# Optimization experiments

Hardware: AMD Instinct MI355X
Metric: run time of the kernel (lower is better)

The kernel has to match this reference:

```python
import jax, jax.numpy as jnp
import numpy as np

B, S, DIN, DOUT = 4, 4096, 768, 768

def setup_inputs() -> dict:
    key = jax.random.key(0)
    kx, kq, kk, kv = jax.random.split(key, 4)
    scale = 1.0 / np.sqrt(DIN)
    return {
        "x": jax.random.normal(kx, (B, S, DIN), dtype=jnp.float32),
        "Wq": jax.random.normal(kq, (DIN, DOUT), dtype=jnp.float32) * scale,
        "Wk": jax.random.normal(kk, (DIN, DOUT), dtype=jnp.float32) * scale,
        "Wv": jax.random.normal(kv, (DIN, DOUT), dtype=jnp.float32) * scale,
    }

def reference(x, Wq, Wk, Wv):
    # q,k,v: [B,S,DOUT]
    q = jnp.einsum('bsd,de->bse', x, Wq)
    k = jnp.einsum('bsd,de->bse', x, Wk)
    v = jnp.einsum('bsd,de->bse', x, Wv)
    # scores: [B,S,S], causal mask (upper triangle -> -inf)
    scores = jnp.einsum('bqe,bke->bqk', q, k)
    causal = jnp.tril(jnp.ones((S, S), dtype=bool))  # True where allowed
    scores = jnp.where(causal[None, :, :], scores, -jnp.inf)
    weights = jax.nn.softmax(scores / jnp.sqrt(jnp.float32(DOUT)), axis=-1)
    # dropout_rate = 0.0 -> identity
    return jnp.einsum('bqk,bke->bqe', weights, v)
```

## Files before the change

kernel.cpp:

```cpp
#include <hip/hip_runtime.h>
#include <math.h>


typedef unsigned short u16;
typedef unsigned int u32;
typedef __attribute__((ext_vector_type(8))) __bf16 bf8;
typedef __attribute__((ext_vector_type(4))) float f32x4;

struct __align__(8) U4 { u16 x, y, z, w; };

#define LOG2E 1.4426950408889634f
#define QSCALE 0.03608439182435161f

#define SBAR() __builtin_amdgcn_s_barrier()
#define WAIT_LGKM0() asm volatile("s_waitcnt lgkmcnt(0)" ::: "memory")
#define WAIT_VM4() asm volatile("s_waitcnt vmcnt(4)" ::: "memory")
#define WAIT_VM0() asm volatile("s_waitcnt vmcnt(0)" ::: "memory")

__device__ __forceinline__ u16 f2bf(float f) {
  u32 u = __builtin_bit_cast(u32, f);
  u += 0x7FFFu + ((u >> 16) & 1u);
  return (u16)(u >> 16);
}
__device__ __forceinline__ f32x4 mfma16(bf8 a, bf8 b, f32x4 c) {
  return __builtin_amdgcn_mfma_f32_16x16x32_bf16(a, b, c, 0, 0, 0);
}
__device__ __forceinline__ void stage16(const void* g, void* l) {
  __builtin_amdgcn_global_load_lds((const __attribute__((address_space(1))) void*)g,
                                   (__attribute__((address_space(3))) void*)l, 16, 0, 0);
}
__device__ __forceinline__ u32 swz7(u32 off) { return off ^ (((off >> 7) & 7u) << 4); }

__global__ void cvt_x_kernel(const float* __restrict__ x, u16* __restrict__ xb) {
  int i = blockIdx.x * 256 + threadIdx.x;
  float4 v = ((const float4*)x)[i];
  U4 o; o.x = f2bf(v.x); o.y = f2bf(v.y); o.z = f2bf(v.z); o.w = f2bf(v.w);
  ((U4*)xb)[i] = o;
}

__global__ void cvt_w_kernel(const float* __restrict__ Wq, const float* __restrict__ Wk,
                             const float* __restrict__ Wv, u16* __restrict__ wt) {
  __shared__ float tile[32][33];
  int z = blockIdx.z;
  const float* W = (z == 0) ? Wq : ((z == 1) ? Wk : Wv);
  u16* o = wt + (size_t)z * 589824;
  int n0 = blockIdx.x * 32, k0 = blockIdx.y * 32;
  int c = threadIdx.x & 31, r0 = threadIdx.x >> 5;
#pragma unroll
  for (int p = 0; p < 4; p++) tile[r0 + p * 8][c] = W[(size_t)(k0 + r0 + p * 8) * 768 + n0 + c];
  __syncthreads();
#pragma unroll
  for (int p = 0; p < 4; p++) o[(size_t)(n0 + r0 + p * 8) * 768 + k0 + c] = f2bf(tile[c][r0 + p * 8]);
}

__global__ __launch_bounds__(256) void gemm_qkv_kernel(
    const u16* __restrict__ xb, const u16* __restrict__ wt,
    u16* __restrict__ qo, u16* __restrict__ ko, u16* __restrict__ vT) {
  __shared__ char lA[16384];
  __shared__ char lB[16384];
  const int tid = threadIdx.x;
  const int lane = tid & 63, wvid = tid >> 6;
  const int wm = wvid >> 1, wn = wvid & 1;
  const int l15 = lane & 15, lg4 = lane >> 4;
  const int m0 = blockIdx.x * 128;
  const int n0 = blockIdx.y * 128;
  const int z = blockIdx.z;
  const u16* wz = wt + (size_t)z * 589824;

  f32x4 acc[4][4];
#pragma unroll
  for (int rt = 0; rt < 4; rt++)
#pragma unroll
    for (int nt = 0; nt < 4; nt++) acc[rt][nt] = f32x4{0.f, 0.f, 0.f, 0.f};

  for (int kt = 0; kt < 12; kt++) {
#pragma unroll
    for (int i = 0; i < 4; i++) {
      u32 o = (u32)i * 4096u + (u32)wvid * 1024u + (u32)lane * 16u;
      u32 lg = swz7(o);
      u32 row = lg >> 7, kbyt = lg & 127u;
      stage16((const char*)xb + ((size_t)(m0 + row) * 1536 + (size_t)kt * 128 + kbyt),
              lA + (size_t)i * 4096 + (size_t)wvid * 1024);
      stage16((const char*)wz + ((size_t)(n0 + row) * 1536 + (size_t)kt * 128 + kbyt),
              lB + (size_t)i * 4096 + (size_t)wvid * 1024);
    }
    __syncthreads();
#pragma unroll
    for (int kk = 0; kk < 2; kk++) {
      bf8 af[4], bfr[4];
#pragma unroll
      for (int rt = 0; rt < 4; rt++) {
        u32 off = (u32)(wm * 64 + rt * 16 + l15) * 128u + (u32)kk * 64u + (u32)lg4 * 16u;
        af[rt] = *(const bf8*)(const void*)(lA + swz7(off));
      }
#pragma unroll
      for (int nt = 0; nt < 4; nt++) {
        u32 off = (u32)(wn * 64 + nt * 16 + l15) * 128u + (u32)kk * 64u + (u32)lg4 * 16u;
        bfr[nt] = *(const bf8*)(const void*)(lB + swz7(off));
      }
#pragma unroll
      for (int rt = 0; rt < 4; rt++)
#pragma unroll
        for (int nt = 0; nt < 4; nt++) acc[rt][nt] = mfma16(af[rt], bfr[nt], acc[rt][nt]);
    }
    __syncthreads();
  }
  if (z == 2) {
#pragma unroll
    for (int rt = 0; rt < 4; rt++) {
      int m = m0 + wm * 64 + rt * 16 + lg4 * 4;
      int batch = m >> 12;
      int s = m & 4095;
#pragma unroll
      for (int nt = 0; nt < 4; nt++) {
        int col = n0 + wn * 64 + nt * 16 + l15;
        U4 pk;
        pk.x = f2bf(acc[rt][nt][0]); pk.y = f2bf(acc[rt][nt][1]);
        pk.z = f2bf(acc[rt][nt][2]); pk.w = f2bf(acc[rt][nt][3]);
        *(U4*)(vT + ((size_t)batch * 768 + col) * 4096 + s) = pk;
      }
    }
  } else {
    u16* dst = (z == 0) ? qo : ko;
    float scl = (z == 0) ? QSCALE : 1.0f;
#pragma unroll
    for (int rt = 0; rt < 4; rt++)
#pragma unroll
      for (int nt = 0; nt < 4; nt++) {
        int col = n0 + wn * 64 + nt * 16 + l15;
#pragma unroll
        for (int j = 0; j < 4; j++) {
          int m = m0 + wm * 64 + rt * 16 + lg4 * 4 + j;
          dst[(size_t)m * 768 + col] = f2bf(acc[rt][nt][j] * scl);
        }
      }
  }
}

__global__ __attribute__((amdgpu_flat_work_group_size(512, 512)))
__attribute__((amdgpu_waves_per_eu(2, 2))) void attn_kernel(
    const u16* __restrict__ qg, const u16* __restrict__ kg, const u16* __restrict__ vg,
    float* __restrict__ out) {
  __shared__ char Qlds[49152];
  __shared__ char Klds[3][32768];
  __shared__ char Plds[8192];
  __shared__ float pm[2][4][16];
  __shared__ float ps[2][4][16];
  __shared__ float mrun[32], lrun[32], alpha_s[32];

  const int tid = threadIdx.x;
  const int lane = tid & 63;
  const int wv = tid >> 6;
  const int rg = wv >> 2;
  const int cg = wv & 3;
  const int l15 = lane & 15, lg4 = lane >> 4;

  const int b = blockIdx.x;
  const int batch = (b >> 1) & 3;
  const int qb_i = 127 - (((b >> 3) << 1) + (b & 1));
  const int qbase = qb_i * 32;
  const size_t boff = (size_t)batch * 4096;
  const int ntile = (qb_i >> 2) + 1;
  const int gtot = ntile * 6;

  const u16* kbase = kg + boff * 768;

  u32 soff[4];
#pragma unroll
  for (int p = 0; p < 4; p++) {
    u32 o = (u32)p * 8192u + (u32)tid * 16u;
    u32 key = o >> 8;
    u32 dbyte = (o & 255u) ^ ((key & 7u) << 4);
    soff[p] = key * 768u + (dbyte >> 1);
  }

#pragma unroll
  for (int p = 0; p < 4; p++)
    stage16(kbase + soff[p], &Klds[0][p * 8192 + tid * 16]);
#pragma unroll
  for (int p = 0; p < 4; p++)
    stage16(kbase + soff[p] + 128u, &Klds[1][p * 8192 + tid * 16]);

#pragma unroll
  for (int j = 0; j < 6; j++) {
    int li = j * 512 + tid;
    int row = li / 96;
    int c16 = li - row * 96;
    int tt = c16 >> 2, sl = c16 & 3;
    u32 daddr = (u32)tt * 2048u + (u32)row * 64u + (u32)((sl ^ ((row >> 1) & 3)) << 4);
    bf8 v = *(const bf8*)(const void*)(qg + (boff + qbase + row) * 768 + c16 * 8);
    *(bf8*)(void*)(Qlds + daddr) = v;
  }
  if (tid < 32) { mrun[tid] = -INFINITY; lrun[tid] = 0.f; }
  WAIT_LGKM0(); SBAR();

  const int qrow_loc = rg * 16 + l15;
  const u32 qlds_base = (u32)qrow_loc * 64u + (u32)((lg4 ^ ((qrow_loc >> 1) & 3)) << 4);
  const u32 kxm = (u32)(l15 & 7) << 4;
  const u32 pa_col = ((u32)lg4 * 16u) ^ ((u32)(l15 & 3) << 4);
  const u32 pa_kx = (u32)((l15 >> 2) & 1);

  f32x4 acc[2][6];
#pragma unroll
  for (int rt = 0; rt < 2; rt++)
#pragma unroll
    for (int ct = 0; ct < 6; ct++) acc[rt][ct] = f32x4{0.f, 0.f, 0.f, 0.f};

  for (int kt = 0; kt < ntile; kt++) {
    const int kb = kt * 128;
    f32x4 sv0 = f32x4{0.f, 0.f, 0.f, 0.f}, sv1 = sv0;

#pragma unroll
    for (int c = 0; c < 6; c++) {
      const int g = kt * 6 + c;
      if (g + 1 < gtot) { WAIT_VM4(); } else { WAIT_VM0(); }
      SBAR();
      {
        const char* kbuf = Klds[c % 3];
#pragma unroll
        for (int ks = 0; ks < 4; ks++) {
          bf8 qv = *(const bf8*)(const void*)(Qlds + qlds_base + (u32)(c * 4 + ks) * 2048u);
          u32 inr = ((u32)ks * 64u + (u32)lg4 * 16u) ^ kxm;
          bf8 kv0 = *(const bf8*)(const void*)(kbuf + (u32)(cg * 32 + l15) * 256u + inr);
          bf8 kv1 = *(const bf8*)(const void*)(kbuf + (u32)(cg * 32 + 16 + l15) * 256u + inr);
          sv0 = mfma16(qv, kv0, sv0);
          sv1 = mfma16(qv, kv1, sv1);
        }
      }
      WAIT_LGKM0(); SBAR();
      if (g + 2 < gtot) {
        const int g2 = g + 2;
        const int kt1 = g2 / 6, c1 = g2 - kt1 * 6;
        const u16* src = kbase + (size_t)(kt1 * 128) * 768 + c1 * 128;
        char* dstb = &Klds[(c + 2) % 3][0];
#pragma unroll
        for (int p = 0; p < 4; p++)
          stage16(src + soff[p], dstb + p * 8192 + tid * 16);
      }
    }

    if (kt == ntile - 1) {
      const int rowg = qbase + rg * 16 + lg4 * 4;
      const int col0 = kb + cg * 32 + l15;
#pragma unroll
      for (int j = 0; j < 4; j++) {
        if (col0 > rowg + j) sv0[j] = -INFINITY;
        if (col0 + 16 > rowg + j) sv1[j] = -INFINITY;
      }
    }
    float rmax[4];
#pragma unroll
    for (int j = 0; j < 4; j++) {
      float m = fmaxf(sv0[j], sv1[j]);
      m = fmaxf(m, __shfl_xor(m, 1));
      m = fmaxf(m, __shfl_xor(m, 2));
      m = fmaxf(m, __shfl_xor(m, 4));
      m = fmaxf(m, __shfl_xor(m, 8));
      rmax[j] = m;
    }
    if (l15 == 0) {
#pragma unroll
      for (int j = 0; j < 4; j++) pm[rg][cg][lg4 * 4 + j] = rmax[j];
    }
    WAIT_LGKM0(); SBAR();
    if (tid < 32) {
      int r2 = tid >> 4, ix = tid & 15;
      float mo = mrun[tid];
      float mn = fmaxf(fmaxf(pm[r2][0][ix], pm[r2][1][ix]), fmaxf(pm[r2][2][ix], pm[r2][3][ix]));
      mn = fmaxf(mo, mn);
      alpha_s[tid] = exp2f((mo - mn) * LOG2E);
      mrun[tid] = mn;
    }
    WAIT_LGKM0(); SBAR();
    {
      float psum[4];
      const int prow0 = rg * 16 + lg4 * 4;
#pragma unroll
      for (int j = 0; j < 4; j++) {
        int r = prow0 + j;
        float mrow = mrun[r];
        float p0 = exp2f((sv0[j] - mrow) * LOG2E);
        float p1 = exp2f((sv1[j] - mrow) * LOG2E);
        u32 rb = (u32)r * 256u;
        u32 msk = (u32)(r & 7) << 4;
        *(u16*)(void*)(Plds + rb + (((u32)(cg * 32 + l15) * 2u) ^ msk)) = f2bf(p0);
        *(u16*)(void*)(Plds + rb + (((u32)(cg * 32 + 16 + l15) * 2u) ^ msk)) = f2bf(p1);
        float su = p0 + p1;
        su += __shfl_xor(su, 1);
        su += __shfl_xor(su, 2);
        su += __shfl_xor(su, 4);
        su += __shfl_xor(su, 8);
        psum[j] = su;
      }
      if (l15 == 0) {
#pragma unroll
        for (int j = 0; j < 4; j++) ps[rg][cg][lg4 * 4 + j] = psum[j];
      }
    }
    const u16* vb0 = vg + ((size_t)batch * 768 + wv * 96 + l15) * 4096 + kb + lg4 * 8;
    bf8 vcur0, vcur1, vcur2, vcur3, vcur4, vcur5;
    vcur0 = *(const bf8*)(const void*)(vb0);
    vcur1 = *(const bf8*)(const void*)(vb0 + 65536);
    vcur2 = *(const bf8*)(const void*)(vb0 + 131072);
    vcur3 = *(const bf8*)(const void*)(vb0 + 196608);
    vcur4 = *(const bf8*)(const void*)(vb0 + 262144);
    vcur5 = *(const bf8*)(const void*)(vb0 + 327680);
    {
      float al[8];
#pragma unroll
      for (int rt = 0; rt < 2; rt++)
#pragma unroll
        for (int j = 0; j < 4; j++) al[rt * 4 + j] = alpha_s[rt * 16 + lg4 * 4 + j];
#pragma unroll
      for (int ct = 0; ct < 6; ct++)
#pragma unroll
        for (int rt = 0; rt < 2; rt++)
#pragma unroll
          for (int j = 0; j < 4; j++) acc[rt][ct][j] *= al[rt * 4 + j];
    }
    WAIT_LGKM0(); SBAR();
    if (tid < 32) {
      int r2 = tid >> 4, ix = tid & 15;
      lrun[tid] = lrun[tid] * alpha_s[tid] +
                  ps[r2][0][ix] + ps[r2][1][ix] + ps[r2][2][ix] + ps[r2][3][ix];
    }
#pragma unroll
    for (int ks = 0; ks < 4; ks++) {
      u32 kss = ((u32)ks ^ pa_kx) * 64u;
      bf8 pa0 = *(const bf8*)(const void*)(Plds + (u32)l15 * 256u + pa_col + kss);
      bf8 pa1 = *(const bf8*)(const void*)(Plds + ((u32)l15 * 256u + 4096u) + pa_col + kss);
      bf8 vn0, vn1, vn2, vn3, vn4, vn5;
      if (ks < 3) {
        const u16* vnp = vb0 + (ks + 1) * 32;
        vn0 = *(const bf8*)(const void*)(vnp);
        vn1 = *(const bf8*)(const void*)(vnp + 65536);
        vn2 = *(const bf8*)(const void*)(vnp + 131072);
        vn3 = *(const bf8*)(const void*)(vnp + 196608);
        vn4 = *(const bf8*)(const void*)(vnp + 262144);
        vn5 = *(const bf8*)(const void*)(vnp + 327680);
      }
      acc[0][0] = mfma16(pa0, vcur0, acc[0][0]);  acc[1][0] = mfma16(pa1, vcur0, acc[1][0]);
      acc[0][1] = mfma16(pa0, vcur1, acc[0][1]);  acc[1][1] = mfma16(pa1, vcur1, acc[1][1]);
      acc[0][2] = mfma16(pa0, vcur2, acc[0][2]);  acc[1][2] = mfma16(pa1, vcur2, acc[1][2]);
      acc[0][3] = mfma16(pa0, vcur3, acc[0][3]);  acc[1][3] = mfma16(pa1, vcur3, acc[1][3]);
      acc[0][4] = mfma16(pa0, vcur4, acc[0][4]);  acc[1][4] = mfma16(pa1, vcur4, acc[1][4]);
      acc[0][5] = mfma16(pa0, vcur5, acc[0][5]);  acc[1][5] = mfma16(pa1, vcur5, acc[1][5]);
      if (ks < 3) {
        vcur0 = vn0; vcur1 = vn1; vcur2 = vn2; vcur3 = vn3; vcur4 = vn4; vcur5 = vn5;
      }
    }
  }
  WAIT_LGKM0(); SBAR();
  float inv[8];
#pragma unroll
  for (int rt = 0; rt < 2; rt++)
#pragma unroll
    for (int j = 0; j < 4; j++) inv[rt * 4 + j] = 1.f / lrun[rt * 16 + lg4 * 4 + j];
#pragma unroll
  for (int ct = 0; ct < 6; ct++)
#pragma unroll
    for (int rt = 0; rt < 2; rt++)
#pragma unroll
      for (int j = 0; j < 4; j++) {
        size_t o = (boff + (size_t)(qbase + rt * 16 + lg4 * 4 + j)) * 768 + wv * 96 + ct * 16 + l15;
        out[o] = acc[rt][ct][j] * inv[rt * 4 + j];
      }
}

extern "C" void kernel_launch(void* const* d_in, const int* in_sizes, int n_in,
                              void* d_out, int out_size, void* d_ws, size_t ws_size,
                              hipStream_t stream) {
  const float* x  = (const float*)d_in[0];
  const float* Wq = (const float*)d_in[1];
  const float* Wk = (const float*)d_in[2];
  const float* Wv = (const float*)d_in[3];
  float* out = (float*)d_out;

  char* ws = (char*)d_ws;
  u16* xb = (u16*)(ws + 256);
  u16* qb = xb + 12582912;
  u16* kb = qb + 12582912;
  u16* vT = kb + 12582912;
  u16* wt = vT + 12582912;

  cvt_x_kernel<<<12288, 256, 0, stream>>>(x, xb);
  cvt_w_kernel<<<dim3(24, 24, 3), 256, 0, stream>>>(Wq, Wk, Wv, wt);
  gemm_qkv_kernel<<<dim3(128, 6, 3), 256, 0, stream>>>(xb, wt, qb, kb, vT);
  attn_kernel<<<512, 512, 0, stream>>>(qb, kb, vT, out);
}
```

Measured before the change: 550.1 us.

## Use 32x32 MFMA for PV, keep Q in registers, widen K chunks

Measured after the change: 611.3 us. 1.11x slower.

```diff
diff --git a/kernel.cpp b/kernel.cpp
--- a/kernel.cpp
+++ b/kernel.cpp
@@ -6,6 +6,7 @@
 typedef unsigned int u32;
 typedef __attribute__((ext_vector_type(8))) __bf16 bf8;
 typedef __attribute__((ext_vector_type(4))) float f32x4;
+typedef __attribute__((ext_vector_type(16))) float f32x16;
 
 struct __align__(8) U4 { u16 x, y, z, w; };
 
@@ -14,7 +15,8 @@
 
 #define SBAR() __builtin_amdgcn_s_barrier()
 #define WAIT_LGKM0() asm volatile("s_waitcnt lgkmcnt(0)" ::: "memory")
-#define WAIT_VM4() asm volatile("s_waitcnt vmcnt(4)" ::: "memory")
+#define WAIT_VM18() asm volatile("s_waitcnt vmcnt(18)" ::: "memory")
+#define WAIT_VM6() asm volatile("s_waitcnt vmcnt(6)" ::: "memory")
 #define WAIT_VM0() asm volatile("s_waitcnt vmcnt(0)" ::: "memory")
 
 __device__ __forceinline__ u16 f2bf(float f) {
@@ -24,6 +26,9 @@
 }
 __device__ __forceinline__ f32x4 mfma16(bf8 a, bf8 b, f32x4 c) {
   return __builtin_amdgcn_mfma_f32_16x16x32_bf16(a, b, c, 0, 0, 0);
+}
+__device__ __forceinline__ f32x16 mfma32(bf8 a, bf8 b, f32x16 c) {
+  return __builtin_amdgcn_mfma_f32_32x32x16_bf16(a, b, c, 0, 0, 0);
 }
 __device__ __forceinline__ void stage16(const void* g, void* l) {
   __builtin_amdgcn_global_load_lds((const __attribute__((address_space(1))) void*)g,
@@ -141,12 +146,11 @@
 __attribute__((amdgpu_waves_per_eu(2, 2))) void attn_kernel(
     const u16* __restrict__ qg, const u16* __restrict__ kg, const u16* __restrict__ vg,
     float* __restrict__ out) {
-  __shared__ char Qlds[49152];
-  __shared__ char Klds[3][32768];
+  __shared__ char Klds[3][49152];
   __shared__ char Plds[8192];
   __shared__ float pm[2][4][16];
   __shared__ float ps[2][4][16];
-  __shared__ float mrun[32], lrun[32], alpha_s[32];
+  __shared__ float mrun_s[32], alpha_s2[32], lrun_s[32];
 
   const int tid = threadIdx.x;
   const int lane = tid & 63;
@@ -154,6 +158,7 @@
   const int rg = wv >> 2;
   const int cg = wv & 3;
   const int l15 = lane & 15, lg4 = lane >> 4;
+  const int l31 = lane & 31, lh = lane >> 5;
 
   const int b = blockIdx.x;
   const int batch = (b >> 1) & 3;
@@ -161,81 +166,78 @@
   const int qbase = qb_i * 32;
   const size_t boff = (size_t)batch * 4096;
   const int ntile = (qb_i >> 2) + 1;
-  const int gtot = ntile * 6;
+  const int gtot = ntile * 4;
 
   const u16* kbase = kg + boff * 768;
 
-  u32 soff[4];
-#pragma unroll
-  for (int p = 0; p < 4; p++) {
+  u32 soff[6];
+#pragma unroll
+  for (int p = 0; p < 6; p++) {
     u32 o = (u32)p * 8192u + (u32)tid * 16u;
-    u32 key = o >> 8;
-    u32 dbyte = (o & 255u) ^ ((key & 7u) << 4);
-    soff[p] = key * 768u + (dbyte >> 1);
-  }
-
-#pragma unroll
-  for (int p = 0; p < 4; p++)
-    stage16(kbase + soff[p], &Klds[0][p * 8192 + tid * 16]);
-#pragma unroll
-  for (int p = 0; p < 4; p++)
-    stage16(kbase + soff[p] + 128u, &Klds[1][p * 8192 + tid * 16]);
-
-#pragma unroll
-  for (int j = 0; j < 6; j++) {
-    int li = j * 512 + tid;
-    int row = li / 96;
-    int c16 = li - row * 96;
-    int tt = c16 >> 2, sl = c16 & 3;
-    u32 daddr = (u32)tt * 2048u + (u32)row * 64u + (u32)((sl ^ ((row >> 1) & 3)) << 4);
-    bf8 v = *(const bf8*)(const void*)(qg + (boff + qbase + row) * 768 + c16 * 8);
-    *(bf8*)(void*)(Qlds + daddr) = v;
-  }
-  if (tid < 32) { mrun[tid] = -INFINITY; lrun[tid] = 0.f; }
+    u32 key = o / 384u;
+    u32 dby = (o - key * 384u) ^ ((key & 7u) << 4);
+    soff[p] = key * 768u + (dby >> 1);
+  }
+
+#pragma unroll
+  for (int p = 0; p < 6; p++) stage16(kbase + soff[p], &Klds[0][p * 8192 + tid * 16]);
+#pragma unroll
+  for (int p = 0; p < 6; p++) stage16(kbase + soff[p] + 192u, &Klds[1][p * 8192 + tid * 16]);
+
+  bf8 qf[24];
+  {
+    const u16* qrow = qg + (boff + qbase + rg * 16 + l15) * 768 + lg4 * 8;
+#pragma unroll
+    for (int t = 0; t < 24; t++) qf[t] = *(const bf8*)(const void*)(qrow + t * 32);
+  }
+  if (tid < 32) { mrun_s[tid] = -INFINITY; lrun_s[tid] = 0.f; }
   WAIT_LGKM0(); SBAR();
 
-  const int qrow_loc = rg * 16 + l15;
-  const u32 qlds_base = (u32)qrow_loc * 64u + (u32)((lg4 ^ ((qrow_loc >> 1) & 3)) << 4);
   const u32 kxm = (u32)(l15 & 7) << 4;
-  const u32 pa_col = ((u32)lg4 * 16u) ^ ((u32)(l15 & 3) << 4);
-  const u32 pa_kx = (u32)((l15 >> 2) & 1);
-
-  f32x4 acc[2][6];
-#pragma unroll
-  for (int rt = 0; rt < 2; rt++)
-#pragma unroll
-    for (int ct = 0; ct < 6; ct++) acc[rt][ct] = f32x4{0.f, 0.f, 0.f, 0.f};
+
+  f32x16 acc0, acc1, acc2;
+#pragma unroll
+  for (int r = 0; r < 16; r++) { acc0[r] = 0.f; acc1[r] = 0.f; acc2[r] = 0.f; }
 
   for (int kt = 0; kt < ntile; kt++) {
     const int kb = kt * 128;
+    const u16* vbase = vg + ((size_t)batch * 768 + wv * 96 + l31) * 4096 + kb + lh * 8;
+    bf8 va[4][3];
+#pragma unroll
+    for (int ks = 0; ks < 4; ks++)
+#pragma unroll
+      for (int ct = 0; ct < 3; ct++)
+        va[ks][ct] = *(const bf8*)(const void*)(vbase + ks * 16 + ct * 131072);
+
     f32x4 sv0 = f32x4{0.f, 0.f, 0.f, 0.f}, sv1 = sv0;
 
 #pragma unroll
-    for (int c = 0; c < 6; c++) {
-      const int g = kt * 6 + c;
-      if (g + 1 < gtot) { WAIT_VM4(); } else { WAIT_VM0(); }
+    for (int c = 0; c < 4; c++) {
+      const int g = kt * 4 + c;
+      if (g + 1 < gtot) { if (c < 2) { WAIT_VM18(); } else { WAIT_VM6(); } }
+      else { WAIT_VM0(); }
       SBAR();
       {
-        const char* kbuf = Klds[c % 3];
-#pragma unroll
-        for (int ks = 0; ks < 4; ks++) {
-          bf8 qv = *(const bf8*)(const void*)(Qlds + qlds_base + (u32)(c * 4 + ks) * 2048u);
+        const char* kbuf = &Klds[g % 3][0];
+        const u32 r0 = (u32)(cg * 32 + l15) * 384u;
+        const u32 r1 = r0 + 16u * 384u;
+#pragma unroll
+        for (int ks = 0; ks < 6; ks++) {
           u32 inr = ((u32)ks * 64u + (u32)lg4 * 16u) ^ kxm;
-          bf8 kv0 = *(const bf8*)(const void*)(kbuf + (u32)(cg * 32 + l15) * 256u + inr);
-          bf8 kv1 = *(const bf8*)(const void*)(kbuf + (u32)(cg * 32 + 16 + l15) * 256u + inr);
-          sv0 = mfma16(qv, kv0, sv0);
-          sv1 = mfma16(qv, kv1, sv1);
+          bf8 kv0 = *(const bf8*)(const void*)(kbuf + r0 + inr);
+          bf8 kv1 = *(const bf8*)(const void*)(kbuf + r1 + inr);
+          sv0 = mfma16(qf[c * 6 + ks], kv0, sv0);
+          sv1 = mfma16(qf[c * 6 + ks], kv1, sv1);
         }
       }
       WAIT_LGKM0(); SBAR();
       if (g + 2 < gtot) {
         const int g2 = g + 2;
-        const int kt1 = g2 / 6, c1 = g2 - kt1 * 6;
-        const u16* src = kbase + (size_t)(kt1 * 128) * 768 + c1 * 128;
-        char* dstb = &Klds[(c + 2) % 3][0];
-#pragma unroll
-        for (int p = 0; p < 4; p++)
-          stage16(src + soff[p], dstb + p * 8192 + tid * 16);
+        const int kt1 = g2 >> 2, c1 = g2 & 3;
+        const u16* src = kbase + (size_t)(kt1 * 128) * 768 + c1 * 192;
+        char* dstb = &Klds[g2 % 3][0];
+#pragma unroll
+        for (int p = 0; p < 6; p++) stage16(src + soff[p], dstb + p * 8192 + tid * 16);
       }
     }
 
@@ -263,22 +265,23 @@
       for (int j = 0; j < 4; j++) pm[rg][cg][lg4 * 4 + j] = rmax[j];
     }
     WAIT_LGKM0(); SBAR();
-    if (tid < 32) {
-      int r2 = tid >> 4, ix = tid & 15;
-      float mo = mrun[tid];
-      float mn = fmaxf(fmaxf(pm[r2][0][ix], pm[r2][1][ix]), fmaxf(pm[r2][2][ix], pm[r2][3][ix]));
+    if (cg == 0 && lg4 == 0) {
+      const int myrow = rg * 16 + l15;
+      float mo = mrun_s[myrow];
+      float mn = fmaxf(fmaxf(pm[rg][0][l15], pm[rg][1][l15]),
+                       fmaxf(pm[rg][2][l15], pm[rg][3][l15]));
       mn = fmaxf(mo, mn);
-      alpha_s[tid] = exp2f((mo - mn) * LOG2E);
-      mrun[tid] = mn;
+      alpha_s2[myrow] = exp2f((mo - mn) * LOG2E);
+      mrun_s[myrow] = mn;
     }
     WAIT_LGKM0(); SBAR();
     {
+      const int prow0 = rg * 16 + lg4 * 4;
       float psum[4];
-      const int prow0 = rg * 16 + lg4 * 4;
 #pragma unroll
       for (int j = 0; j < 4; j++) {
-        int r = prow0 + j;
-        float mrow = mrun[r];
+        const int r = prow0 + j;
+        const float mrow = mrun_s[r];
         float p0 = exp2f((sv0[j] - mrow) * LOG2E);
         float p1 = exp2f((sv1[j] - mrow) * LOG2E);
         u32 rb = (u32)r * 256u;
@@ -297,74 +300,45 @@
         for (int j = 0; j < 4; j++) ps[rg][cg][lg4 * 4 + j] = psum[j];
       }
     }
-    const u16* vb0 = vg + ((size_t)batch * 768 + wv * 96 + l15) * 4096 + kb + lg4 * 8;
-    bf8 vcur0, vcur1, vcur2, vcur3, vcur4, vcur5;
-    vcur0 = *(const bf8*)(const void*)(vb0);
-    vcur1 = *(const bf8*)(const void*)(vb0 + 65536);
-    vcur2 = *(const bf8*)(const void*)(vb0 + 131072);
-    vcur3 = *(const bf8*)(const void*)(vb0 + 196608);
-    vcur4 = *(const bf8*)(const void*)(vb0 + 262144);
-    vcur5 = *(const bf8*)(const void*)(vb0 + 327680);
     {
-      float al[8];
-#pragma unroll
-      for (int rt = 0; rt < 2; rt++)
-#pragma unroll
-        for (int j = 0; j < 4; j++) al[rt * 4 + j] = alpha_s[rt * 16 + lg4 * 4 + j];
-#pragma unroll
-      for (int ct = 0; ct < 6; ct++)
-#pragma unroll
-        for (int rt = 0; rt < 2; rt++)
-#pragma unroll
-          for (int j = 0; j < 4; j++) acc[rt][ct][j] *= al[rt * 4 + j];
+      float al[16];
+#pragma unroll
+      for (int r = 0; r < 16; r++) al[r] = alpha_s2[(r & 3) + 8 * (r >> 2) + 4 * lh];
+#pragma unroll
+      for (int r = 0; r < 16; r++) { acc0[r] *= al[r]; acc1[r] *= al[r]; acc2[r] *= al[r]; }
     }
     WAIT_LGKM0(); SBAR();
-    if (tid < 32) {
-      int r2 = tid >> 4, ix = tid & 15;
-      lrun[tid] = lrun[tid] * alpha_s[tid] +
-                  ps[r2][0][ix] + ps[r2][1][ix] + ps[r2][2][ix] + ps[r2][3][ix];
-    }
-#pragma unroll
-    for (int ks = 0; ks < 4; ks++) {
-      u32 kss = ((u32)ks ^ pa_kx) * 64u;
-      bf8 pa0 = *(const bf8*)(const void*)(Plds + (u32)l15 * 256u + pa_col + kss);
-      bf8 pa1 = *(const bf8*)(const void*)(Plds + ((u32)l15 * 256u + 4096u) + pa_col + kss);
-      bf8 vn0, vn1, vn2, vn3, vn4, vn5;
-      if (ks < 3) {
-        const u16* vnp = vb0 + (ks + 1) * 32;
-        vn0 = *(const bf8*)(const void*)(vnp);
-        vn1 = *(const bf8*)(const void*)(vnp + 65536);
-        vn2 = *(const bf8*)(const void*)(vnp + 131072);
-        vn3 = *(const bf8*)(const void*)(vnp + 196608);
-        vn4 = *(const bf8*)(const void*)(vnp + 262144);
-        vn5 = *(const bf8*)(const void*)(vnp + 327680);
-      }
-      acc[0][0] = mfma16(pa0, vcur0, acc[0][0]);  acc[1][0] = mfma16(pa1, vcur0, acc[1][0]);
-      acc[0][1] = mfma16(pa0, vcur1, acc[0][1]);  acc[1][1] = mfma16(pa1, vcur1, acc[1][1]);
-      acc[0][2] = mfma16(pa0, vcur2, acc[0][2]);  acc[1][2] = mfma16(pa1, vcur2, acc[1][2]);
-      acc[0][3] = mfma16(pa0, vcur3, acc[0][3]);  acc[1][3] = mfma16(pa1, vcur3, acc[1][3]);
-      acc[0][4] = mfma16(pa0, vcur4, acc[0][4]);  acc[1][4] = mfma16(pa1, vcur4, acc[1][4]);
-      acc[0][5] = mfma16(pa0, vcur5, acc[0][5]);  acc[1][5] = mfma16(pa1, vcur5, acc[1][5]);
-      if (ks < 3) {
-        vcur0 = vn0; vcur1 = vn1; vcur2 = vn2; vcur3 = vn3; vcur4 = vn4; vcur5 = vn5;
+    if (cg == 0 && lg4 == 0) {
+      const int myrow = rg * 16 + l15;
+      lrun_s[myrow] = lrun_s[myrow] * alpha_s2[myrow] +
+                      ps[rg][0][l15] + ps[rg][1][l15] + ps[rg][2][l15] + ps[rg][3][l15];
+    }
+#pragma unroll
+    for (int ks = 0; ks < 8; ks++) {
+      u32 paddr = (u32)l31 * 256u + ((((u32)ks * 32u + (u32)lh * 16u)) ^ (((u32)(l31 & 7)) << 4));
+      bf8 pa = *(const bf8*)(const void*)(Plds + paddr);
+      acc0 = mfma32(pa, va[ks & 3][0], acc0);
+      acc1 = mfma32(pa, va[ks & 3][1], acc1);
+      acc2 = mfma32(pa, va[ks & 3][2], acc2);
+      if (ks < 4) {
+#pragma unroll
+        for (int ct = 0; ct < 3; ct++)
+          va[ks][ct] = *(const bf8*)(const void*)(vbase + (ks + 4) * 16 + ct * 131072);
       }
     }
   }
   WAIT_LGKM0(); SBAR();
-  float inv[8];
-#pragma unroll
-  for (int rt = 0; rt < 2; rt++)
-#pragma unroll
-    for (int j = 0; j < 4; j++) inv[rt * 4 + j] = 1.f / lrun[rt * 16 + lg4 * 4 + j];
-#pragma unroll
-  for (int ct = 0; ct < 6; ct++)
-#pragma unroll
-    for (int rt = 0; rt < 2; rt++)
-#pragma unroll
-      for (int j = 0; j < 4; j++) {
-        size_t o = (boff + (size_t)(qbase + rt * 16 + lg4 * 4 + j)) * 768 + wv * 96 + ct * 16 + l15;
-        out[o] = acc[rt][ct][j] * inv[rt * 4 + j];
-      }
+  float inv[16];
+#pragma unroll
+  for (int r = 0; r < 16; r++) inv[r] = 1.f / lrun_s[(r & 3) + 8 * (r >> 2) + 4 * lh];
+#pragma unroll
+  for (int r = 0; r < 16; r++) {
+    const int row = (r & 3) + 8 * (r >> 2) + 4 * lh;
+    size_t o = (boff + (size_t)(qbase + row)) * 768 + wv * 96 + l31;
+    out[o] = acc0[r] * inv[r];
+    out[o + 32] = acc1[r] * inv[r];
+    out[o + 64] = acc2[r] * inv[r];
+  }
 }
 
 extern "C" void kernel_launch(void* const* d_in, const int* in_sizes, int n_in,
```
